# Kernel tuning notes

Measured on AMD Instinct MI355X. Metric: run time of the kernel, lower is better.

## Reference

```python
import jax, jax.numpy as jnp
import numpy as np

D_MODEL = 1024
NUM_HEADS = 16
D_K = D_MODEL // NUM_HEADS
ROPE_THETA = 10000.0


def _rope(x, positions):
    # x: [B, H, S, Dk]; positions: [S] int. Interleaved-pair RoPE, theta=10000.
    half = D_K // 2
    inv_freq = 1.0 / (ROPE_THETA ** (jnp.arange(half, dtype=jnp.float32) * 2.0 / D_K))
    ang = positions.astype(jnp.float32)[:, None] * inv_freq[None, :]  # [S, half]
    cos = jnp.cos(ang)[None, None]  # [1,1,S,half]
    sin = jnp.sin(ang)[None, None]
    x_even = x[..., 0::2]
    x_odd = x[..., 1::2]
    r_even = x_even * cos - x_odd * sin
    r_odd = x_even * sin + x_odd * cos
    out = jnp.stack([r_even, r_odd], axis=-1)  # [B,H,S,half,2]
    return out.reshape(x.shape)


def setup_inputs() -> dict:
    key = jax.random.key(0)
    ks = jax.random.split(key, 5)
    B, S = 4, 2048
    std = (2.0 / (D_MODEL + D_MODEL)) ** 0.5
    return {
        "x": jax.random.normal(ks[0], (B, S, D_MODEL), dtype=jnp.float32),
        "Wq": jax.random.normal(ks[1], (D_MODEL, D_MODEL), dtype=jnp.float32) * std,
        "Wk": jax.random.normal(ks[2], (D_MODEL, D_MODEL), dtype=jnp.float32) * std,
        "Wv": jax.random.normal(ks[3], (D_MODEL, D_MODEL), dtype=jnp.float32) * std,
        "Wo": jax.random.normal(ks[4], (D_MODEL, D_MODEL), dtype=jnp.float32) * std,
        "token_positions": jnp.arange(S, dtype=jnp.int32),
    }


def reference(x, Wq, Wk, Wv, Wo, token_positions):
    B, S, _ = x.shape
    # QKV projections (weights stored [out, in], y = x @ W^T)
    def proj(W):
        y = jnp.einsum('bsi,oi->bso', x, W)
        return y.reshape(B, S, NUM_HEADS, D_K).transpose(0, 2, 1, 3)  # [B,H,S,Dk]
    q = _rope(proj(Wq), token_positions)
    k = _rope(proj(Wk), token_positions)
    v = proj(Wv)
    scores = jnp.einsum('bhqd,bhkd->bhqk', q, k) / jnp.sqrt(jnp.float32(D_K))
    causal = token_positions[:, None] >= token_positions[None, :]  # [S,S]
    scores = jnp.where(causal[None, None], scores, jnp.float32(-1e9))
    probs = jax.nn.softmax(scores, axis=-1)
    attn = jnp.einsum('bhqk,bhkd->bhqd', probs, v)
    attn = attn.transpose(0, 2, 1, 3).reshape(B, S, D_MODEL)
    return jnp.einsum('bsi,oi->bso', attn, Wo)
```

## Files before the change

kernel.cpp:

```cpp
#include <hip/hip_runtime.h>
#include <hip/hip_bf16.h>
#include <math.h>

#define SEQ 2048
#define BATCH 4
#define MROWS (BATCH*SEQ)
#define DMODEL 1024
#define NHEADS 16
#define DKH 64

typedef float f32x4 __attribute__((ext_vector_type(4)));
typedef float f32x16 __attribute__((ext_vector_type(16)));
typedef __bf16 bf16x8 __attribute__((ext_vector_type(8)));
typedef unsigned short u16;
typedef unsigned int u32;
typedef u16 u16x4 __attribute__((ext_vector_type(4)));
typedef u16 u16x8 __attribute__((ext_vector_type(8)));
typedef u32 u32x4v __attribute__((ext_vector_type(4)));

__device__ __forceinline__ u16 f2bf(float f) {
  union { float f; unsigned u; } v; v.f = f;
  unsigned r = v.u + 0x7FFFu + ((v.u >> 16) & 1u);
  return (u16)(r >> 16);
}

__device__ __forceinline__ void async_copy16(const void* g, void* l) {
  __builtin_amdgcn_global_load_lds(
      (const __attribute__((address_space(1))) void*)g,
      (__attribute__((address_space(3))) void*)l, 16, 0, 0);
}

__device__ __forceinline__ u32 cvtpk(float lo, float hi) {
  u32 r;
  asm("v_cvt_pk_bf16_f32 %0, %1, %2" : "=v"(r) : "v"(lo), "v"(hi));
  return r;
}

__global__ __launch_bounds__(256) void k_prep(
    const float* __restrict__ x,
    const float* __restrict__ Wq, const float* __restrict__ Wk,
    const float* __restrict__ Wv, const float* __restrict__ Wo,
    const int* __restrict__ pos,
    u16* __restrict__ xb, u16* __restrict__ Wqb, u16* __restrict__ Wkb,
    u16* __restrict__ Wvb, u16* __restrict__ Wob,
    float2* __restrict__ csT)
{
  const int bid = blockIdx.x, tid = threadIdx.x;
  if (bid < 8192) {
    int i = bid*256 + tid;
    float4 v = ((const float4*)x)[i];
    u16x4 o; o[0]=f2bf(v.x); o[1]=f2bf(v.y); o[2]=f2bf(v.z); o[3]=f2bf(v.w);
    ((u16x4*)xb)[i] = o;
  } else if (bid < 12288) {
    int wi = (bid - 8192) >> 10;
    const float* src = (wi==0)?Wq:(wi==1)?Wk:(wi==2)?Wv:Wo;
    u16* dst = (wi==0)?Wqb:(wi==1)?Wkb:(wi==2)?Wvb:Wob;
    int i = ((bid - 8192) & 1023)*256 + tid;
    float4 v = ((const float4*)src)[i];
    u16x4 o; o[0]=f2bf(v.x); o[1]=f2bf(v.y); o[2]=f2bf(v.z); o[3]=f2bf(v.w);
    ((u16x4*)dst)[i] = o;
  } else {
    int i = (bid - 12288)*256 + tid;
    int s = i >> 5, j = i & 31;
    double p = (double)pos[s];
    double inv = pow(10000.0, -(double)j / 32.0);
    double a = p * inv;
    csT[i] = make_float2((float)cos(a), (float)sin(a));
  }
}

template<int MODE>
__global__ __launch_bounds__(256) void k_g3(
    const u16* __restrict__ A,
    const u16* __restrict__ W0, const u16* __restrict__ W1,
    const u16* __restrict__ W2,
    u16* __restrict__ Qo, u16* __restrict__ Ko, u16* __restrict__ Vto,
    float* __restrict__ Fo,
    const float2* __restrict__ csT)
{
  __shared__ alignas(16) u16 As[128*64];
  __shared__ alignas(16) u16 Bs[128*64];

  const int bm = blockIdx.x, y = blockIdx.y;
  int proj, bnl;
  const u16* W;
  if constexpr (MODE == 0) {
    proj = y >> 3; bnl = y & 7;
    W = (proj == 0) ? W0 : (proj == 1) ? W1 : W2;
  } else {
    proj = 3; bnl = y; W = W0;
  }

  const int tid = threadIdx.x;
  const int wave = tid >> 6, lane = tid & 63;
  const int lg = lane >> 4, lr = lane & 15;
  const int wm = wave >> 1, wn = wave & 1;

  const u16* Ab = A + (size_t)(bm*128)*DMODEL;
  const u16* Wb = W + (size_t)(bnl*128)*DMODEL;

  f32x4 acc[4][4];
#pragma unroll
  for (int i = 0; i < 4; ++i)
#pragma unroll
    for (int j = 0; j < 4; ++j) acc[i][j] = (f32x4){0,0,0,0};

  for (int t = 0; t < 16; ++t) {
    const int k0 = t * 64;
#pragma unroll
    for (int i = 0; i < 4; ++i) {
      const int idx = i*256 + tid;
      const int row = idx >> 3, ch = idx & 7;
      const int sc = (ch ^ (row & 7)) * 8;
      async_copy16(Ab + (size_t)row*DMODEL + k0 + sc, (char*)As + idx*16);
      async_copy16(Wb + (size_t)row*DMODEL + k0 + sc, (char*)Bs + idx*16);
    }
    __syncthreads();
#pragma unroll
    for (int kk = 0; kk < 2; ++kk) {
      bf16x8 bfr[4];
#pragma unroll
      for (int ni = 0; ni < 4; ++ni) {
        const int row = wn*64 + ni*16 + lr;
        bfr[ni] = *(const bf16x8*)&Bs[row*64 + (((kk*4 + lg) ^ (row & 7)) * 8)];
      }
#pragma unroll
      for (int mi = 0; mi < 4; ++mi) {
        const int row = wm*64 + mi*16 + lr;
        bf16x8 af = *(const bf16x8*)&As[row*64 + (((kk*4 + lg) ^ (row & 7)) * 8)];
#pragma unroll
        for (int ni = 0; ni < 4; ++ni)
          acc[mi][ni] = __builtin_amdgcn_mfma_f32_16x16x32_bf16(af, bfr[ni], acc[mi][ni], 0, 0, 0);
      }
    }
    __syncthreads();
  }

#pragma unroll
  for (int mi = 0; mi < 4; ++mi) {
    const int row0 = bm*128 + wm*64 + mi*16 + lg*4;
#pragma unroll
    for (int ni = 0; ni < 4; ++ni) {
      const int col = bnl*128 + wn*64 + ni*16 + lr;
      f32x4 a = acc[mi][ni];
      if constexpr (MODE == 1) {
#pragma unroll
        for (int r = 0; r < 4; ++r) Fo[(size_t)(row0+r)*DMODEL + col] = a[r];
      } else {
        if (proj == 2) {
          const int hh = col >> 6, dd = col & 63;
          const int s0r = row0 & (SEQ-1);
          const int bb = row0 >> 11;
          u16x4 wv;
#pragma unroll
          for (int r = 0; r < 4; ++r) wv[r] = f2bf(a[r]);
          *(u16x4*)&Vto[((size_t)((bb*16+hh)*64 + dd))*SEQ + s0r] = wv;
        } else {
          u16* C = (proj == 0) ? Qo : Ko;
          const float scl = (proj == 0) ? 0.18033688f : 1.0f;
          const int dd = col & 63;
          const int jj = dd >> 1;
          const float sgn = (dd & 1) ? 1.0f : -1.0f;
#pragma unroll
          for (int r = 0; r < 4; ++r) {
            const int s = (row0 + r) & (SEQ-1);
            float v = a[r];
            float pv = __shfl_xor(v, 1, 64);
            float2 cs = csT[s*32 + jj];
            C[(size_t)(row0+r)*DMODEL + col] = f2bf((v*cs.x + sgn*pv*cs.y) * scl);
          }
        }
      }
    }
  }
}

__global__ __launch_bounds__(512) void k_attn(
    const u16* __restrict__ Q, const u16* __restrict__ K,
    const u16* __restrict__ Vt, u16* __restrict__ O)
{
  const int B = blockIdx.x;
  const int bh = ((B & 7) << 3) | ((B >> 3) & 7);
  const int qt = 7 - (B >> 6);
  const int b = bh >> 4, h = bh & 15;
  const int wave = threadIdx.x >> 6, lane = threadIdx.x & 63;
  const int ql = lane & 31, hi = lane >> 5, hi4 = hi * 4;
  const int R0 = qt*256 + wave*32;

  __shared__ alignas(16) u16 Ks[2][64*64];
  __shared__ alignas(16) u16 Vs[2][64*64];

  const u16* Qb = Q + (size_t)(b*SEQ)*DMODEL + h*64;
  const u16* Kb = K + (size_t)(b*SEQ)*DMODEL + h*64;
  const u16* Vb = Vt + (size_t)(bh*64)*SEQ;

  bf16x8 qf[4];
#pragma unroll
  for (int j = 0; j < 4; ++j)
    qf[j] = *(const bf16x8*)(Qb + (size_t)(R0 + ql)*DMODEL + j*16 + hi*8);

  union { u16x8 u; bf16x8 v; } onesu;
#pragma unroll
  for (int i = 0; i < 8; ++i) onesu.u[i] = 0x3F80;
  const bf16x8 ones = onesu.v;

  f32x16 o0 = (f32x16)(0.f), o1 = (f32x16)(0.f);
  f32x16 lacc = (f32x16)(0.f);
  float m_run = -INFINITY;
  const float THR2 = 11.5415603f;

  const int KT = (qt + 1) * 4;
  const int qp = (ql & ~12) | ((ql & 4) << 1) | ((ql & 8) >> 1);

  auto stage = [&](int buf, int kt) {
    const int idx = threadIdx.x;
    const int row = idx >> 3, ch = idx & 7;
    const int sch = (ch ^ (row & 7)) * 8;
    const int k0 = kt * 64;
    async_copy16(Kb + (size_t)(k0 + row)*DMODEL + sch, (char*)Ks[buf] + idx*16);
    async_copy16(Vb + (size_t)row*SEQ + k0 + sch,      (char*)Vs[buf] + idx*16);
  };

  stage(0, 0);
  __syncthreads();

  for (int kt = 0; kt < KT; ++kt) {
    const int cur = kt & 1;
    if (kt + 1 < KT) stage(cur ^ 1, kt + 1);

    const int k0 = kt*64;
    if (k0 <= R0 + 31) {
      const u16* Kw = Ks[cur];
      const u16* Vw = Vs[cur];

      bf16x8 ka[2][4];
#pragma unroll
      for (int st = 0; st < 2; ++st)
#pragma unroll
        for (int j = 0; j < 4; ++j) {
          const int rk = st*32 + qp;
          const int c = (2*j + hi) ^ (rk & 7);
          ka[st][j] = *(const bf16x8*)&Kw[rk*64 + c*8];
        }
      f32x16 s0 = (f32x16)(0.f), s1 = (f32x16)(0.f);
#pragma unroll
      for (int j = 0; j < 4; ++j) {
        s0 = __builtin_amdgcn_mfma_f32_32x32x16_bf16(ka[0][j], qf[j], s0, 0, 0, 0);
        s1 = __builtin_amdgcn_mfma_f32_32x32x16_bf16(ka[1][j], qf[j], s1, 0, 0, 0);
      }

      if (k0 + 63 > R0) {
        const int base = k0 - R0;
#pragma unroll
        for (int r = 0; r < 16; ++r) {
          const int kl = (r & 7) + (hi << 3) + ((r & 8) << 1);
          s0[r] = (ql >= base + kl)      ? s0[r] : -1e30f;
          s1[r] = (ql >= base + 32 + kl) ? s1[r] : -1e30f;
        }
      }

      float t[16];
#pragma unroll
      for (int r = 0; r < 16; ++r) t[r] = fmaxf(s0[r], s1[r]);
#pragma unroll
      for (int w = 8; w >= 1; w >>= 1)
#pragma unroll
        for (int r = 0; r < w; ++r) t[r] = fmaxf(t[r], t[r+w]);
      const float mx = fmaxf(t[0], __shfl_xor(t[0], 32, 64));

      if (__any(mx > m_run + THR2)) {
        const float mn = fmaxf(m_run, mx);
        const float al = __builtin_exp2f(m_run - mn);
        m_run = mn;
        lacc[0] *= al;
#pragma unroll
        for (int r = 0; r < 16; ++r) { o0[r] *= al; o1[r] *= al; }
      }

      float e0[16], e1[16];
#pragma unroll
      for (int r = 0; r < 16; ++r) {
        e0[r] = __builtin_exp2f(s0[r] - m_run);
        e1[r] = __builtin_exp2f(s1[r] - m_run);
      }

      bf16x8 pb[4];
#pragma unroll
      for (int sl = 0; sl < 4; ++sl) {
        const float* e = (sl < 2) ? e0 : e1;
        const int o8 = (sl & 1) * 8;
        u32 w0 = cvtpk(e[o8+0], e[o8+1]);
        u32 w1 = cvtpk(e[o8+2], e[o8+3]);
        u32 w2 = cvtpk(e[o8+4], e[o8+5]);
        u32 w3 = cvtpk(e[o8+6], e[o8+7]);
        union { u32x4v u; bf16x8 v; } uu;
        uu.u = (u32x4v){w0, w1, w2, w3};
        pb[sl] = uu.v;
      }

#pragma unroll
      for (int sl = 0; sl < 4; ++sl) {
        const int c0 = 2*sl + hi;
        const int d0 = ql,      ca = (c0 ^ (d0 & 7));
        const int d1 = 32 + ql, cb = (c0 ^ (d1 & 7));
        bf16x8 va0 = *(const bf16x8*)&Vw[d0*64 + ca*8];
        bf16x8 va1 = *(const bf16x8*)&Vw[d1*64 + cb*8];
        o0 = __builtin_amdgcn_mfma_f32_32x32x16_bf16(va0, pb[sl], o0, 0, 0, 0);
        o1 = __builtin_amdgcn_mfma_f32_32x32x16_bf16(va1, pb[sl], o1, 0, 0, 0);
        lacc = __builtin_amdgcn_mfma_f32_32x32x16_bf16(ones, pb[sl], lacc, 0, 0, 0);
      }
    }
    __syncthreads();
  }

  const float inv = 1.0f / lacc[0];
  u16* Orow = O + (size_t)(b*SEQ + R0 + ql)*DMODEL + h*64;
#pragma unroll
  for (int rb = 0; rb < 4; ++rb) {
    u16x4 wA, wB;
#pragma unroll
    for (int j = 0; j < 4; ++j) {
      wA[j] = f2bf(o0[rb*4 + j] * inv);
      wB[j] = f2bf(o1[rb*4 + j] * inv);
    }
    *(u16x4*)(Orow + 8*rb + hi4)      = wA;
    *(u16x4*)(Orow + 32 + 8*rb + hi4) = wB;
  }
}

extern "C" void kernel_launch(void* const* d_in, const int* in_sizes, int n_in,
                              void* d_out, int out_size, void* d_ws, size_t ws_size,
                              hipStream_t stream) {
  const float* x  = (const float*)d_in[0];
  const float* Wq = (const float*)d_in[1];
  const float* Wk = (const float*)d_in[2];
  const float* Wv = (const float*)d_in[3];
  const float* Wo = (const float*)d_in[4];
  const int* pos  = (const int*)d_in[5];
  float* out = (float*)d_out;

  const size_t SZ_X   = (size_t)MROWS*DMODEL*2;
  const size_t SZ_W   = (size_t)DMODEL*DMODEL*2;
  const size_t SZ_TAB = (size_t)SEQ*32*8;
  char* w = (char*)d_ws;
  u16* xb   = (u16*)(w);
  u16* Wqb  = (u16*)(w + SZ_X);
  u16* Wkb  = (u16*)(w + SZ_X + SZ_W);
  u16* Wvb  = (u16*)(w + SZ_X + 2*SZ_W);
  u16* Wob  = (u16*)(w + SZ_X + 3*SZ_W);
  float2* csT = (float2*)(w + SZ_X + 4*SZ_W);
  u16* Qb   = (u16*)(w + SZ_X + 4*SZ_W + SZ_TAB);
  u16* Kb   = (u16*)(w + 2*SZ_X + 4*SZ_W + SZ_TAB);
  u16* Ob   = (u16*)(w + 3*SZ_X + 4*SZ_W + SZ_TAB);
  u16* Vt   = (u16*)(w + 4*SZ_X + 4*SZ_W + SZ_TAB);
  const size_t need = 5*SZ_X + 4*SZ_W + SZ_TAB;
  if (ws_size < need) return;

  k_prep<<<12544, 256, 0, stream>>>(x, Wq, Wk, Wv, Wo, pos,
                                    xb, Wqb, Wkb, Wvb, Wob, csT);
  k_g3<0><<<dim3(64, 24), 256, 0, stream>>>(
      xb, Wqb, Wkb, Wvb, Qb, Kb, Vt, nullptr, csT);
  k_attn<<<512, 512, 0, stream>>>(Qb, Kb, Vt, Ob);
  k_g3<1><<<dim3(64, 8), 256, 0, stream>>>(
      Ob, Wob, nullptr, nullptr, nullptr, nullptr, nullptr, out, csT);
}
```

Measured before the change: 194.9 us.

## Stage QKV projection epilogue through shared memory for coalesced 16-byte stores

The QKV GEMM epilogue now writes RoPE-rotated bf16 results into a swizzled 128x128 shared-memory tile, reusing the A/B staging buffers, and then stores them with coalesced 16-byte vector writes. For V, the transposed layout is produced by gathering from shared memory, replacing the scattered 8-byte stores. Before, Q and K were written one 2-byte element at a time with poor coalescing. The RoPE table setup also switches from double-precision pow/cos/sin to fast float exp2 and intrinsics, which lowers the cost of the prep kernel but may lose accuracy at large angles.

```diff
diff --git a/kernel.cpp b/kernel.cpp
--- a/kernel.cpp
+++ b/kernel.cpp
@@ -62,10 +62,10 @@
   } else {
     int i = (bid - 12288)*256 + tid;
     int s = i >> 5, j = i & 31;
-    double p = (double)pos[s];
-    double inv = pow(10000.0, -(double)j / 32.0);
-    double a = p * inv;
-    csT[i] = make_float2((float)cos(a), (float)sin(a));
+    float p = (float)pos[s];
+    float inv = __builtin_exp2f((float)j * -0.4152410118f);
+    float a = p * inv;
+    csT[i] = make_float2(__cosf(a), __sinf(a));
   }
 }
 
@@ -78,8 +78,9 @@
     float* __restrict__ Fo,
     const float2* __restrict__ csT)
 {
-  __shared__ alignas(16) u16 As[128*64];
-  __shared__ alignas(16) u16 Bs[128*64];
+  __shared__ alignas(16) u16 smem[128*128];
+  u16* Asl = smem;
+  u16* Bsl = smem + 128*64;
 
   const int bm = blockIdx.x, y = blockIdx.y;
   int proj, bnl;
@@ -112,8 +113,8 @@
       const int idx = i*256 + tid;
       const int row = idx >> 3, ch = idx & 7;
       const int sc = (ch ^ (row & 7)) * 8;
-      async_copy16(Ab + (size_t)row*DMODEL + k0 + sc, (char*)As + idx*16);
-      async_copy16(Wb + (size_t)row*DMODEL + k0 + sc, (char*)Bs + idx*16);
+      async_copy16(Ab + (size_t)row*DMODEL + k0 + sc, (char*)Asl + idx*16);
+      async_copy16(Wb + (size_t)row*DMODEL + k0 + sc, (char*)Bsl + idx*16);
     }
     __syncthreads();
 #pragma unroll
@@ -122,12 +123,12 @@
 #pragma unroll
       for (int ni = 0; ni < 4; ++ni) {
         const int row = wn*64 + ni*16 + lr;
-        bfr[ni] = *(const bf16x8*)&Bs[row*64 + (((kk*4 + lg) ^ (row & 7)) * 8)];
+        bfr[ni] = *(const bf16x8*)&Bsl[row*64 + (((kk*4 + lg) ^ (row & 7)) * 8)];
       }
 #pragma unroll
       for (int mi = 0; mi < 4; ++mi) {
         const int row = wm*64 + mi*16 + lr;
-        bf16x8 af = *(const bf16x8*)&As[row*64 + (((kk*4 + lg) ^ (row & 7)) * 8)];
+        bf16x8 af = *(const bf16x8*)&Asl[row*64 + (((kk*4 + lg) ^ (row & 7)) * 8)];
 #pragma unroll
         for (int ni = 0; ni < 4; ++ni)
           acc[mi][ni] = __builtin_amdgcn_mfma_f32_16x16x32_bf16(af, bfr[ni], acc[mi][ni], 0, 0, 0);
@@ -136,40 +137,78 @@
     __syncthreads();
   }
 
-#pragma unroll
-  for (int mi = 0; mi < 4; ++mi) {
-    const int row0 = bm*128 + wm*64 + mi*16 + lg*4;
-#pragma unroll
-    for (int ni = 0; ni < 4; ++ni) {
-      const int col = bnl*128 + wn*64 + ni*16 + lr;
-      f32x4 a = acc[mi][ni];
-      if constexpr (MODE == 1) {
+  if constexpr (MODE == 1) {
+#pragma unroll
+    for (int mi = 0; mi < 4; ++mi) {
+      const int row0 = bm*128 + wm*64 + mi*16 + lg*4;
+#pragma unroll
+      for (int ni = 0; ni < 4; ++ni) {
+        const int col = bnl*128 + wn*64 + ni*16 + lr;
+        f32x4 a = acc[mi][ni];
 #pragma unroll
         for (int r = 0; r < 4; ++r) Fo[(size_t)(row0+r)*DMODEL + col] = a[r];
-      } else {
-        if (proj == 2) {
-          const int hh = col >> 6, dd = col & 63;
-          const int s0r = row0 & (SEQ-1);
-          const int bb = row0 >> 11;
-          u16x4 wv;
-#pragma unroll
-          for (int r = 0; r < 4; ++r) wv[r] = f2bf(a[r]);
-          *(u16x4*)&Vto[((size_t)((bb*16+hh)*64 + dd))*SEQ + s0r] = wv;
-        } else {
-          u16* C = (proj == 0) ? Qo : Ko;
-          const float scl = (proj == 0) ? 0.18033688f : 1.0f;
-          const int dd = col & 63;
-          const int jj = dd >> 1;
-          const float sgn = (dd & 1) ? 1.0f : -1.0f;
-#pragma unroll
-          for (int r = 0; r < 4; ++r) {
-            const int s = (row0 + r) & (SEQ-1);
+      }
+    }
+  } else {
+    u16* Ct = smem;
+#pragma unroll
+    for (int mi = 0; mi < 4; ++mi) {
+#pragma unroll
+      for (int ni = 0; ni < 4; ++ni) {
+        const int col = wn*64 + ni*16 + lr;
+        f32x4 a = acc[mi][ni];
+#pragma unroll
+        for (int r = 0; r < 4; ++r) {
+          const int row = wm*64 + mi*16 + lg*4 + r;
+          float val;
+          if (proj == 2) {
+            val = a[r];
+          } else {
+            const float scl = (proj == 0) ? 0.18033688f : 1.0f;
+            const int dd = col & 63;
+            const int jj = dd >> 1;
+            const float sgn = (dd & 1) ? 1.0f : -1.0f;
+            const int s = (bm*128 + row) & (SEQ-1);
             float v = a[r];
             float pv = __shfl_xor(v, 1, 64);
             float2 cs = csT[s*32 + jj];
-            C[(size_t)(row0+r)*DMODEL + col] = f2bf((v*cs.x + sgn*pv*cs.y) * scl);
+            val = (v*cs.x + sgn*pv*cs.y) * scl;
           }
+          const int c = col >> 3, k = (row >> 3) & 7;
+          Ct[row*128 + (((c ^ k) << 3) | (col & 7))] = f2bf(val);
         }
+      }
+    }
+    __syncthreads();
+
+    if (proj != 2) {
+      u16* C = (proj == 0) ? Qo : Ko;
+#pragma unroll
+      for (int i = 0; i < 8; ++i) {
+        const int idx = i*256 + tid;
+        const int row = idx >> 4;
+        const int ch  = idx & 15;
+        u16x8 v = *(const u16x8*)&Ct[row*128 + ((ch ^ ((row >> 3) & 7)) << 3)];
+        *(u16x8*)&C[(size_t)(bm*128 + row)*DMODEL + bnl*128 + ch*8] = v;
+      }
+    } else {
+      const int bb = (bm*128) >> 11;
+      const int s0 = (bm*128) & (SEQ-1);
+#pragma unroll
+      for (int i = 0; i < 8; ++i) {
+        const int idx = i*256 + tid;
+        const int col = idx >> 4;
+        const int sch = idx & 15;
+        const int c = col >> 3;
+        u16x8 v;
+#pragma unroll
+        for (int j = 0; j < 8; ++j) {
+          const int row = sch*8 + j;
+          v[j] = Ct[row*128 + (((c ^ ((row >> 3) & 7)) << 3) | (col & 7))];
+        }
+        const int gc = bnl*128 + col;
+        const int hh = gc >> 6, dd = gc & 63;
+        *(u16x8*)&Vto[((size_t)((bb*16 + hh)*64 + dd))*SEQ + s0 + sch*8] = v;
       }
     }
   }
```

New measurement: 205.0 us. +5.2%, slower.
